# Optimization experiments

Hardware: AMD Instinct MI355X
Metric: run time of the kernel (lower is better)

## Reference

```python
import jax, jax.numpy as jnp
import numpy as np

N_NODES = 50000
N_EDGES = 800000
IN_C, HID_C, OUT_C = 128, 128, 64


def setup_inputs() -> dict:
    key = jax.random.key(0)
    k_x, k_e, k_w1, k_w2 = jax.random.split(key, 4)
    x = jax.random.normal(k_x, (N_NODES, IN_C), dtype=jnp.float32)
    edge_index = jax.random.randint(k_e, (2, N_EDGES), 0, N_NODES, dtype=jnp.int64)
    # Glorot-style scaled weights (as in PyG GCNConv linear layers)
    W1 = jax.random.normal(k_w1, (IN_C, HID_C), dtype=jnp.float32) * (1.0 / np.sqrt(IN_C))
    b1 = jnp.zeros((HID_C,), dtype=jnp.float32)
    W2 = jax.random.normal(k_w2, (HID_C, OUT_C), dtype=jnp.float32) * (1.0 / np.sqrt(HID_C))
    b2 = jnp.zeros((OUT_C,), dtype=jnp.float32)
    return {"x": x, "edge_index": edge_index, "W1": W1, "b1": b1, "W2": W2, "b2": b2}


def _gcn_norm(edge_index, num_nodes):
    """Add self-loops and compute symmetric D^{-1/2} A D^{-1/2} edge coefficients."""
    loop = jnp.arange(num_nodes, dtype=edge_index.dtype)
    src = jnp.concatenate([edge_index[0], loop])  # [E + N]
    dst = jnp.concatenate([edge_index[1], loop])  # [E + N]
    w = jnp.ones(src.shape[0], dtype=jnp.float32)  # edge_weight=None -> ones
    deg = jax.ops.segment_sum(w, dst, num_segments=num_nodes)  # includes self-loop
    dinv = jnp.where(deg > 0, jax.lax.rsqrt(deg), 0.0)
    norm = dinv[src] * w * dinv[dst]  # [E + N]
    return src, dst, norm


def _gcn_conv(h, W, b, src, dst, norm, num_nodes):
    h = h @ W                               # [N, out] dense transform
    msg = h[src] * norm[:, None]            # [E+N, out] gather + scale
    agg = jax.ops.segment_sum(msg, dst, num_segments=num_nodes)  # scatter-add
    return agg + b


def reference(x, edge_index, W1, b1, W2, b2):
    n = x.shape[0]
    src, dst, norm = _gcn_norm(edge_index, n)
    h = _gcn_conv(x, W1, b1, src, dst, norm, n)
    h = jax.nn.relu(h)
    # dropout p=0.5 is identity in eval mode (training=False)
    return _gcn_conv(h, W2, b2, src, dst, norm, n)
```

## Files before the change

### kernel.cpp

```cpp
#include <hip/hip_runtime.h>

#define C_IN  128
#define C_HID 128
#define C_OUT 64
#define TILE  4096

typedef __attribute__((ext_vector_type(8))) short short8;
typedef __attribute__((ext_vector_type(4))) float f32x4;

__device__ __forceinline__ unsigned f2bf(float f) {
    unsigned u = __float_as_uint(f);
    return (u + 0x7FFF + ((u >> 16) & 1)) >> 16;
}
__device__ __forceinline__ float bflo(unsigned t) { return __uint_as_float(t << 16); }
__device__ __forceinline__ float bfhi(unsigned t) { return __uint_as_float(t & 0xFFFF0000u); }


__global__ __launch_bounds__(256) void k_cvt(const float4* __restrict__ in, uint2* __restrict__ outp, int n4) {
    int i = blockIdx.x * 256 + threadIdx.x;
    if (i < n4) {
        float4 v = in[i];
        uint2 o;
        o.x = (f2bf(v.y) << 16) | f2bf(v.x);
        o.y = (f2bf(v.w) << 16) | f2bf(v.z);
        outp[i] = o;
    }
}


__global__ __launch_bounds__(256) void k_histo(const int* __restrict__ ei, int* __restrict__ histT,
                                               int E, int NT, int NB) {
    __shared__ int h[256];
    const int t = blockIdx.x;
    const int tid = threadIdx.x;
    h[tid] = 0;
    __syncthreads();
    const int end = min((t + 1) * TILE, E);
    for (int i = t * TILE + tid; i < end; i += 256)
        atomicAdd(&h[ei[E + i] >> 8], 1);
    __syncthreads();
    if (tid < NB) histT[tid * NT + t] = h[tid];
}

__global__ __launch_bounds__(256) void k_scan1(const int* __restrict__ in, int* __restrict__ outp,
                                               int* __restrict__ bsum, int n) {
    __shared__ int s[256];
    int tid = threadIdx.x;
    int i = blockIdx.x * 256 + tid;
    int v = (i < n) ? in[i] : 0;
    s[tid] = v;
    __syncthreads();
    #pragma unroll
    for (int off = 1; off < 256; off <<= 1) {
        int t = (tid >= off) ? s[tid - off] : 0;
        __syncthreads();
        s[tid] += t;
        __syncthreads();
    }
    if (i < n) outp[i] = s[tid] - v;
    if (tid == 255) bsum[blockIdx.x] = s[255];
}

__global__ __launch_bounds__(256) void k_scan2(const int* __restrict__ bsum, int* __restrict__ bpre, int nb) {
    __shared__ int s[256];
    int tid = threadIdx.x;
    int v = (tid < nb) ? bsum[tid] : 0;
    s[tid] = v;
    __syncthreads();
    #pragma unroll
    for (int off = 1; off < 256; off <<= 1) {
        int t = (tid >= off) ? s[tid - off] : 0;
        __syncthreads();
        s[tid] += t;
        __syncthreads();
    }
    if (tid < nb) bpre[tid] = s[tid] - v;
}

__global__ __launch_bounds__(256) void k_scanAdd(int* __restrict__ outp, const int* __restrict__ bpre, int n) {
    int i = blockIdx.x * 256 + threadIdx.x;
    if (i < n) outp[i] += bpre[blockIdx.x];
}

__global__ __launch_bounds__(256) void k_reorder(const int* __restrict__ ei,
                                                 const int* __restrict__ tileOff,
                                                 unsigned* __restrict__ tmp,
                                                 int E, int NT, int NB) {
    __shared__ int cur[256];
    const int t = blockIdx.x;
    const int tid = threadIdx.x;
    if (tid < NB) cur[tid] = tileOff[tid * NT + t];
    __syncthreads();
    const int end = min((t + 1) * TILE, E);
    for (int i = t * TILE + tid; i < end; i += 256) {
        int d = ei[E + i];
        int s = ei[i];
        int p = atomicAdd(&cur[d >> 8], 1);
        tmp[p] = ((unsigned)s << 8) | (unsigned)(d & 255);
    }
}

__global__ __launch_bounds__(256) void k_bucket(const unsigned* __restrict__ tmp,
                                                const int* __restrict__ tileOff,
                                                int* __restrict__ row_ptr,
                                                float* __restrict__ dinv,
                                                int* __restrict__ csr_src,
                                                int E, int NT, int NB, int n) {
    __shared__ int c[256], ssc[256], lcur[256];
    const int b = blockIdx.x;
    const int tid = threadIdx.x;
    const int rbeg = tileOff[b * NT];
    const int rend = (b + 1 < NB) ? tileOff[(b + 1) * NT] : E;

    c[tid] = 0;
    __syncthreads();
    for (int i = rbeg + tid; i < rend; i += 256)
        atomicAdd(&c[tmp[i] & 255], 1);
    __syncthreads();

    ssc[tid] = c[tid];
    __syncthreads();
    #pragma unroll
    for (int off = 1; off < 256; off <<= 1) {
        int t2 = (tid >= off) ? ssc[tid - off] : 0;
        __syncthreads();
        ssc[tid] += t2;
        __syncthreads();
    }
    const int ex = ssc[tid] - c[tid];

    const int d = b * 256 + tid;
    if (d < n) {
        row_ptr[d] = rbeg + ex;
        dinv[d] = rsqrtf((float)(c[tid] + 1));
        if (d == n - 1) row_ptr[n] = E;
    }
    lcur[tid] = rbeg + ex;
    __syncthreads();

    for (int i = rbeg + tid; i < rend; i += 256) {
        unsigned w = tmp[i];
        int p = atomicAdd(&lcur[w & 255], 1);
        csr_src[p] = (int)(w >> 8);
    }
}


template<int N>
__global__ __launch_bounds__(256) void k_gemm_mfma(const unsigned short* __restrict__ X,
                                                   const float* __restrict__ W,
                                                   const float* __restrict__ dinv,
                                                   unsigned short* __restrict__ H, int M) {
    constexpr int K = 128;
    constexpr int LDT = K + 8;
    __shared__ unsigned short sWt[N * LDT];

    const int tid = threadIdx.x;
    constexpr int NLOG = (N == 128) ? 7 : 6;
    for (int idx = tid; idx < K * N; idx += 256) {
        int k = idx >> NLOG, c = idx & (N - 1);
        sWt[c * LDT + k] = (unsigned short)f2bf(W[idx]);
    }
    __syncthreads();

    const int wave = __builtin_amdgcn_readfirstlane(tid >> 6);
    const int lane = tid & 63;
    const int m0 = blockIdx.x * 64 + wave * 16;
    if (m0 >= M) return;

    const int arow = lane & 15;
    const int koff = (lane >> 4) * 8;

    const unsigned short* ap = X + (size_t)(m0 + arow) * K + koff;
    short8 a[4];
    #pragma unroll
    for (int q = 0; q < 4; ++q) a[q] = *(const short8*)(ap + q * 32);

    const int row0 = m0 + (lane >> 4) * 4;
    const float4 dv = *(const float4*)(dinv + row0);

    #pragma unroll
    for (int ct = 0; ct < N / 16; ++ct) {
        const int bcol = ct * 16 + (lane & 15);
        const unsigned short* bp = &sWt[bcol * LDT + koff];
        f32x4 acc = {0.f, 0.f, 0.f, 0.f};
        #pragma unroll
        for (int q = 0; q < 4; ++q) {
            short8 bq = *(const short8*)(bp + q * 32);
            acc = __builtin_amdgcn_mfma_f32_16x16x32_bf16(a[q], bq, acc, 0, 0, 0);
        }
        const int col = ct * 16 + (lane & 15);
        #pragma unroll
        for (int r = 0; r < 4; ++r) {
            float dr = (r == 0) ? dv.x : (r == 1) ? dv.y : (r == 2) ? dv.z : dv.w;
            H[(size_t)(row0 + r) * N + col] = (unsigned short)f2bf(acc[r] * dr);
        }
    }
}


template<int C, bool RELU, bool OUTBF>
__global__ __launch_bounds__(256) void k_agg(const void* __restrict__ hraw,
                                             const int* __restrict__ row_ptr,
                                             const int* __restrict__ csr_src,
                                             const float* __restrict__ dinv,
                                             const float* __restrict__ bias,
                                             void* __restrict__ agg, int n) {
    constexpr int U = 16;
    constexpr int VPC = C / 64;
    const int lane = threadIdx.x & 63;
    const int wv = __builtin_amdgcn_readfirstlane(threadIdx.x >> 6);
    const int v = blockIdx.x * 4 + wv;
    if (v >= n) return;

    const unsigned*       hu = (const unsigned*)hraw;
    const unsigned short* hs = (const unsigned short*)hraw;

    const int e0 = row_ptr[v], e1 = row_ptr[v + 1];
    const float dd = dinv[v];

    float acc[VPC];
    if (VPC == 2) {
        unsigned t = hu[(size_t)v * 64 + lane];
        acc[0] = bflo(t);
        acc[1] = bfhi(t);
    } else {
        acc[0] = bflo(hs[(size_t)v * 64 + lane]);
    }

    int j0 = e0;
    for (; j0 + U <= e1; j0 += U) {
        int ss[U];
        #pragma unroll
        for (int u = 0; u < U; ++u) ss[u] = csr_src[j0 + u];
        float hv[U][VPC];
        #pragma unroll
        for (int u = 0; u < U; ++u) {
            if (VPC == 2) {
                unsigned t = hu[(size_t)ss[u] * 64 + lane];
                hv[u][0] = bflo(t);
                hv[u][1] = bfhi(t);
            } else {
                hv[u][0] = bflo(hs[(size_t)ss[u] * 64 + lane]);
            }
        }
        #pragma unroll
        for (int u = 0; u < U; ++u) {
            acc[0] += hv[u][0];
            if (VPC == 2) acc[1] += hv[u][1];
        }
    }
    if (j0 < e1) {
        int ss[U];
        #pragma unroll
        for (int u = 0; u < U; ++u) {
            int sraw = csr_src[j0 + u];
            ss[u] = (j0 + u < e1) ? sraw : v;
        }
        float hv[U][VPC];
        #pragma unroll
        for (int u = 0; u < U; ++u) {
            if (VPC == 2) {
                unsigned t = hu[(size_t)ss[u] * 64 + lane];
                hv[u][0] = bflo(t);
                hv[u][1] = bfhi(t);
            } else {
                hv[u][0] = bflo(hs[(size_t)ss[u] * 64 + lane]);
            }
        }
        #pragma unroll
        for (int u = 0; u < U; ++u) {
            float m = (j0 + u < e1) ? 1.f : 0.f;
            acc[0] = fmaf(m, hv[u][0], acc[0]);
            if (VPC == 2) acc[1] = fmaf(m, hv[u][1], acc[1]);
        }
    }

    if (VPC == 2) {
        float2 bv = ((const float2*)bias)[lane];
        float ox = acc[0] * dd + bv.x;
        float oy = acc[1] * dd + bv.y;
        if (RELU) { ox = fmaxf(ox, 0.f); oy = fmaxf(oy, 0.f); }
        if (OUTBF) {
            ((unsigned*)agg)[(size_t)v * 64 + lane] = (f2bf(oy) << 16) | f2bf(ox);
        } else {
            ((float2*)agg)[(size_t)v * 64 + lane] = make_float2(ox, oy);
        }
    } else {
        float o = acc[0] * dd + bias[lane];
        if (RELU) o = fmaxf(o, 0.f);
        if (OUTBF) ((unsigned short*)agg)[(size_t)v * 64 + lane] = (unsigned short)f2bf(o);
        else       ((float*)agg)[(size_t)v * 64 + lane] = o;
    }
}


extern "C" void kernel_launch(void* const* d_in, const int* in_sizes, int n_in,
                              void* d_out, int out_size, void* d_ws, size_t ws_size,
                              hipStream_t stream) {
    const float* x  = (const float*)d_in[0];
    const int*   ei = (const int*)d_in[1];
    const float* W1 = (const float*)d_in[2];
    const float* b1 = (const float*)d_in[3];
    const float* W2 = (const float*)d_in[4];
    const float* b2 = (const float*)d_in[5];
    float* out = (float*)d_out;

    const int N = in_sizes[0] / C_IN;
    const int E = in_sizes[1] / 2;
    const int NT = (E + TILE - 1) / TILE;
    const int NB = (N + 255) >> 8;
    const int M2 = NB * NT;

    char* base = (char*)d_ws;
    size_t off = 0;
    auto alloc = [&](size_t bytes) {
        char* q = base + off;
        off = (off + bytes + 15) & ~(size_t)15;
        return q;
    };
    int*   histT    = (int*)  alloc((size_t)M2 * 4);
    int*   tileOff  = (int*)  alloc((size_t)M2 * 4);
    int*   bsumH    = (int*)  alloc(256 * 4);
    int*   bpreH    = (int*)  alloc(256 * 4);
    unsigned* tmp   = (unsigned*)alloc((size_t)E * 4);
    int*   row_ptr  = (int*)  alloc((size_t)(N + 1) * 4);
    float* dinv     = (float*)alloc((size_t)N * 4);
    int*   csr_src  = (int*)  alloc((size_t)E * 4);
    unsigned short* xb   = (unsigned short*)alloc((size_t)N * C_IN * 2);
    unsigned short* h    = (unsigned short*)alloc((size_t)N * C_HID * 2);
    unsigned short* agg1 = (unsigned short*)alloc((size_t)N * C_HID * 2);
    unsigned short* h2   = h;

    dim3 blk(256);
    const int nbS2 = (M2 + 255) / 256;

    k_cvt<<<((N * C_IN / 4) + 255) / 256, blk, 0, stream>>>((const float4*)x, (uint2*)xb, N * C_IN / 4);

    k_histo  <<<NT, blk, 0, stream>>>(ei, histT, E, NT, NB);
    k_scan1  <<<nbS2, blk, 0, stream>>>(histT, tileOff, bsumH, M2);
    k_scan2  <<<1, blk, 0, stream>>>(bsumH, bpreH, nbS2);
    k_scanAdd<<<nbS2, blk, 0, stream>>>(tileOff, bpreH, M2);
    k_reorder<<<NT, blk, 0, stream>>>(ei, tileOff, tmp, E, NT, NB);
    k_bucket <<<NB, blk, 0, stream>>>(tmp, tileOff, row_ptr, dinv, csr_src, E, NT, NB, N);

    const int gblocks = (N + 63) / 64;
    const int ablocks = (N + 3) / 4;

    k_gemm_mfma<C_HID><<<gblocks, blk, 0, stream>>>(xb, W1, dinv, h, N);
    k_agg<C_HID, true, true><<<ablocks, blk, 0, stream>>>(h, row_ptr, csr_src, dinv, b1, agg1, N);

    k_gemm_mfma<C_OUT><<<gblocks, blk, 0, stream>>>(agg1, W2, dinv, h2, N);
    k_agg<C_OUT, false, false><<<ablocks, blk, 0, stream>>>(h2, row_ptr, csr_src, dinv, b2, out, N);
}
```

Baseline: 124.0 us.

## Fuse cvt with histogram and collapse three-pass scan into per-bucket tile scan

```diff
diff --git a/kernel.cpp b/kernel.cpp
--- a/kernel.cpp
+++ b/kernel.cpp
@@ -15,39 +15,8 @@
 __device__ __forceinline__ float bflo(unsigned t) { return __uint_as_float(t << 16); }
 __device__ __forceinline__ float bfhi(unsigned t) { return __uint_as_float(t & 0xFFFF0000u); }
 
-
-__global__ __launch_bounds__(256) void k_cvt(const float4* __restrict__ in, uint2* __restrict__ outp, int n4) {
-    int i = blockIdx.x * 256 + threadIdx.x;
-    if (i < n4) {
-        float4 v = in[i];
-        uint2 o;
-        o.x = (f2bf(v.y) << 16) | f2bf(v.x);
-        o.y = (f2bf(v.w) << 16) | f2bf(v.z);
-        outp[i] = o;
-    }
-}
-
-
-__global__ __launch_bounds__(256) void k_histo(const int* __restrict__ ei, int* __restrict__ histT,
-                                               int E, int NT, int NB) {
-    __shared__ int h[256];
-    const int t = blockIdx.x;
-    const int tid = threadIdx.x;
-    h[tid] = 0;
-    __syncthreads();
-    const int end = min((t + 1) * TILE, E);
-    for (int i = t * TILE + tid; i < end; i += 256)
-        atomicAdd(&h[ei[E + i] >> 8], 1);
-    __syncthreads();
-    if (tid < NB) histT[tid * NT + t] = h[tid];
-}
-
-__global__ __launch_bounds__(256) void k_scan1(const int* __restrict__ in, int* __restrict__ outp,
-                                               int* __restrict__ bsum, int n) {
-    __shared__ int s[256];
-    int tid = threadIdx.x;
-    int i = blockIdx.x * 256 + tid;
-    int v = (i < n) ? in[i] : 0;
+__device__ __forceinline__ int block_exscan(int v, int* s) {
+    const int tid = threadIdx.x;
     s[tid] = v;
     __syncthreads();
     #pragma unroll
@@ -57,60 +26,88 @@
         s[tid] += t;
         __syncthreads();
     }
-    if (i < n) outp[i] = s[tid] - v;
-    if (tid == 255) bsum[blockIdx.x] = s[255];
-}
-
-__global__ __launch_bounds__(256) void k_scan2(const int* __restrict__ bsum, int* __restrict__ bpre, int nb) {
+    return s[tid] - v;
+}
+
+
+__global__ __launch_bounds__(256) void k_cvt_histo(const float4* __restrict__ in, uint2* __restrict__ outp,
+                                                   int n4, const int* __restrict__ ei,
+                                                   int* __restrict__ histT, int E, int NT, int NB) {
+    const int tid = threadIdx.x;
+    if ((int)blockIdx.x < NT) {
+        __shared__ int h[256];
+        const int t = blockIdx.x;
+        h[tid] = 0;
+        __syncthreads();
+        const int end = min((t + 1) * TILE, E);
+        for (int i = t * TILE + tid; i < end; i += 256)
+            atomicAdd(&h[ei[E + i] >> 8], 1);
+        __syncthreads();
+        if (tid < NB) histT[tid * NT + t] = h[tid];
+    } else {
+        int i = ((int)blockIdx.x - NT) * 256 + tid;
+        if (i < n4) {
+            float4 v = in[i];
+            uint2 o;
+            o.x = (f2bf(v.y) << 16) | f2bf(v.x);
+            o.y = (f2bf(v.w) << 16) | f2bf(v.z);
+            outp[i] = o;
+        }
+    }
+}
+
+
+__global__ __launch_bounds__(256) void k_tilescan(const int* __restrict__ histT,
+                                                  int* __restrict__ tilePrefix,
+                                                  int* __restrict__ BT, int NT, int NB) {
     __shared__ int s[256];
-    int tid = threadIdx.x;
-    int v = (tid < nb) ? bsum[tid] : 0;
-    s[tid] = v;
-    __syncthreads();
-    #pragma unroll
-    for (int off = 1; off < 256; off <<= 1) {
-        int t = (tid >= off) ? s[tid - off] : 0;
-        __syncthreads();
-        s[tid] += t;
-        __syncthreads();
-    }
-    if (tid < nb) bpre[tid] = s[tid] - v;
-}
-
-__global__ __launch_bounds__(256) void k_scanAdd(int* __restrict__ outp, const int* __restrict__ bpre, int n) {
-    int i = blockIdx.x * 256 + threadIdx.x;
-    if (i < n) outp[i] += bpre[blockIdx.x];
-}
+    const int b = blockIdx.x;
+    const int tid = threadIdx.x;
+    int v = (tid < NT) ? histT[b * NT + tid] : 0;
+    int ex = block_exscan(v, s);
+    if (tid < NT) tilePrefix[b * NT + tid] = ex;
+    if (tid == 255) BT[b] = s[255];
+}
+
 
 __global__ __launch_bounds__(256) void k_reorder(const int* __restrict__ ei,
-                                                 const int* __restrict__ tileOff,
+                                                 const int* __restrict__ tilePrefix,
+                                                 const int* __restrict__ BT,
                                                  unsigned* __restrict__ tmp,
                                                  int E, int NT, int NB) {
+    __shared__ int s[256];
     __shared__ int cur[256];
     const int t = blockIdx.x;
     const int tid = threadIdx.x;
-    if (tid < NB) cur[tid] = tileOff[tid * NT + t];
+    int v = (tid < NB) ? BT[tid] : 0;
+    int base = block_exscan(v, s);
+    if (tid < NB) cur[tid] = base + tilePrefix[tid * NT + t];
     __syncthreads();
     const int end = min((t + 1) * TILE, E);
     for (int i = t * TILE + tid; i < end; i += 256) {
         int d = ei[E + i];
-        int s = ei[i];
+        int sv = ei[i];
         int p = atomicAdd(&cur[d >> 8], 1);
-        tmp[p] = ((unsigned)s << 8) | (unsigned)(d & 255);
-    }
-}
+        tmp[p] = ((unsigned)sv << 8) | (unsigned)(d & 255);
+    }
+}
+
 
 __global__ __launch_bounds__(256) void k_bucket(const unsigned* __restrict__ tmp,
-                                                const int* __restrict__ tileOff,
+                                                const int* __restrict__ BT,
                                                 int* __restrict__ row_ptr,
                                                 float* __restrict__ dinv,
                                                 int* __restrict__ csr_src,
-                                                int E, int NT, int NB, int n) {
-    __shared__ int c[256], ssc[256], lcur[256];
+                                                int E, int NB, int n) {
+    __shared__ int sA[256], c[256], ssc[256], lcur[256];
     const int b = blockIdx.x;
     const int tid = threadIdx.x;
-    const int rbeg = tileOff[b * NT];
-    const int rend = (b + 1 < NB) ? tileOff[(b + 1) * NT] : E;
+
+    int v = (tid < NB) ? BT[tid] : 0;
+    (void)block_exscan(v, sA);
+    const int vb = BT[b];
+    const int rbeg = sA[b] - vb;
+    const int rend = rbeg + vb;
 
     c[tid] = 0;
     __syncthreads();
@@ -118,16 +115,7 @@
         atomicAdd(&c[tmp[i] & 255], 1);
     __syncthreads();
 
-    ssc[tid] = c[tid];
-    __syncthreads();
-    #pragma unroll
-    for (int off = 1; off < 256; off <<= 1) {
-        int t2 = (tid >= off) ? ssc[tid - off] : 0;
-        __syncthreads();
-        ssc[tid] += t2;
-        __syncthreads();
-    }
-    const int ex = ssc[tid] - c[tid];
+    int ex = block_exscan(c[tid], ssc);
 
     const int d = b * 256 + tid;
     if (d < n) {
@@ -319,30 +307,27 @@
         off = (off + bytes + 15) & ~(size_t)15;
         return q;
     };
-    int*   histT    = (int*)  alloc((size_t)M2 * 4);
-    int*   tileOff  = (int*)  alloc((size_t)M2 * 4);
-    int*   bsumH    = (int*)  alloc(256 * 4);
-    int*   bpreH    = (int*)  alloc(256 * 4);
-    unsigned* tmp   = (unsigned*)alloc((size_t)E * 4);
-    int*   row_ptr  = (int*)  alloc((size_t)(N + 1) * 4);
-    float* dinv     = (float*)alloc((size_t)N * 4);
-    int*   csr_src  = (int*)  alloc((size_t)E * 4);
+    int*   histT      = (int*)  alloc((size_t)M2 * 4);
+    int*   tilePrefix = (int*)  alloc((size_t)M2 * 4);
+    int*   BT         = (int*)  alloc(256 * 4);
+    unsigned* tmp     = (unsigned*)alloc((size_t)E * 4);
+    int*   row_ptr    = (int*)  alloc((size_t)(N + 1) * 4);
+    float* dinv       = (float*)alloc((size_t)N * 4);
+    int*   csr_src    = (int*)  alloc((size_t)E * 4);
     unsigned short* xb   = (unsigned short*)alloc((size_t)N * C_IN * 2);
     unsigned short* h    = (unsigned short*)alloc((size_t)N * C_HID * 2);
     unsigned short* agg1 = (unsigned short*)alloc((size_t)N * C_HID * 2);
     unsigned short* h2   = h;
 
     dim3 blk(256);
-    const int nbS2 = (M2 + 255) / 256;
-
-    k_cvt<<<((N * C_IN / 4) + 255) / 256, blk, 0, stream>>>((const float4*)x, (uint2*)xb, N * C_IN / 4);
-
-    k_histo  <<<NT, blk, 0, stream>>>(ei, histT, E, NT, NB);
-    k_scan1  <<<nbS2, blk, 0, stream>>>(histT, tileOff, bsumH, M2);
-    k_scan2  <<<1, blk, 0, stream>>>(bsumH, bpreH, nbS2);
-    k_scanAdd<<<nbS2, blk, 0, stream>>>(tileOff, bpreH, M2);
-    k_reorder<<<NT, blk, 0, stream>>>(ei, tileOff, tmp, E, NT, NB);
-    k_bucket <<<NB, blk, 0, stream>>>(tmp, tileOff, row_ptr, dinv, csr_src, E, NT, NB, N);
+    const int n4 = N * C_IN / 4;
+    const int cvtBlocks = (n4 + 255) / 256;
+
+    k_cvt_histo<<<NT + cvtBlocks, blk, 0, stream>>>((const float4*)x, (uint2*)xb, n4,
+                                                    ei, histT, E, NT, NB);
+    k_tilescan<<<NB, blk, 0, stream>>>(histT, tilePrefix, BT, NT, NB);
+    k_reorder<<<NT, blk, 0, stream>>>(ei, tilePrefix, BT, tmp, E, NT, NB);
+    k_bucket<<<NB, blk, 0, stream>>>(tmp, BT, row_ptr, dinv, csr_src, E, NB, N);
 
     const int gblocks = (N + 63) / 64;
     const int ablocks = (N + 3) / 4;
```

Result: faster. 118.2 us (-4.7%).
